# Kernel optimization log

Measured on AMD Instinct MI355X. Metric: run time of the kernel, lower is better.

The kernel has to match this reference:

```python
import jax, jax.numpy as jnp
import numpy as np

N = 50000
IN_C, HID, OUT_C = 128, 64, 40


def setup_inputs() -> dict:
    key = jax.random.key(0)
    ks = jax.random.split(key, 10)
    x = jax.random.normal(ks[0], (N, IN_C), dtype=jnp.float32)
    edge_index = jax.random.randint(ks[1], (2, 1600000), 0, N, dtype=jnp.int64)
    edge_attr = jax.random.uniform(ks[2], (1600000,), dtype=jnp.float32)
    def lin(k, fan_in, fan_out):
        bound = 1.0 / np.sqrt(fan_in)
        return jax.random.uniform(k, (fan_in, fan_out), jnp.float32, -bound, bound)
    W1 = lin(ks[3], IN_C, HID); b1 = jnp.zeros((HID,), jnp.float32)
    W2 = lin(ks[4], HID, HID); b2 = jnp.zeros((HID,), jnp.float32)
    W3 = lin(ks[5], HID, OUT_C); b3 = jnp.zeros((OUT_C,), jnp.float32)
    return {"x": x, "edge_index": edge_index, "edge_attr": edge_attr,
            "W1": W1, "b1": b1, "W2": W2, "b2": b2, "W3": W3, "b3": b3}


def _gcn_conv(x, src, dst, norm, W, b):
    # h = x W ; out[i] = sum_{(j->i)} norm_e * h[j] ; + bias
    h = x @ W
    msg = norm[:, None] * h[src]          # [E+N, F_out] gathered messages
    out = jax.ops.segment_sum(msg, dst, num_segments=N)
    return out + b


def reference(x, edge_index, edge_attr, W1, b1, W2, b2, W3, b3):
    # GCN normalization with self-loops (fill_value=1), cached across layers.
    loops = jnp.arange(N, dtype=edge_index.dtype)
    src = jnp.concatenate([edge_index[0], loops])
    dst = jnp.concatenate([edge_index[1], loops])
    w = jnp.concatenate([edge_attr, jnp.ones((N,), edge_attr.dtype)])
    deg = jnp.zeros((N,), x.dtype).at[dst].add(w)
    dinv = jnp.where(deg > 0, jax.lax.rsqrt(deg), 0.0)
    norm = dinv[src] * w * dinv[dst]

    h = jax.nn.relu(_gcn_conv(x, src, dst, norm, W1, b1))   # dropout: eval no-op
    h = jax.nn.relu(_gcn_conv(h, src, dst, norm, W2, b2))
    h = jax.nn.relu(_gcn_conv(h, src, dst, norm, W3, b3))
    return jax.nn.log_softmax(h, axis=-1)
```

## Files before the change

kernel.cpp:

```cpp
#include <hip/hip_runtime.h>
#include <math.h>

#define N_NODES 50000
#define E_EDGES 1600000
#define IN_C    128
#define HID     64
#define OUT_C   40

#define BSH     9
#define BNODES  512
#define NB      98
#define CAP     20480
#define TILE    4096
#define P1T     512
#define NPB     16

typedef unsigned int uint;
typedef unsigned short ushort;

__device__ inline float b2f(ushort h) { return __uint_as_float(((uint)h) << 16); }
__device__ inline ushort f2b(float f) {
    uint u = __float_as_uint(f);
    u += 0x7FFFu + ((u >> 16) & 1u);
    return (ushort)(u >> 16);
}

__global__ __launch_bounds__(P1T) void k_bin(const int* __restrict__ ei,
                                             const float* __restrict__ w,
                                             int* __restrict__ bcursor,
                                             uint2* __restrict__ tmp) {
    __shared__ uint2 stage[TILE];
    __shared__ unsigned char sbuck[TILE];
    __shared__ int hist[NB], startb[NB], cursor[NB], baseg[NB];
    __shared__ int sc[128];
    const int tid = threadIdx.x;
    const int e0  = blockIdx.x * TILE;
    const int n   = min(TILE, E_EDGES - e0);

    for (int i = tid; i < NB; i += P1T) hist[i] = 0;
    __syncthreads();

    for (int i = tid; i < n; i += P1T) {
        int d = ei[E_EDGES + e0 + i];
        atomicAdd(&hist[d >> BSH], 1);
    }
    __syncthreads();

    if (tid < 128) sc[tid] = (tid < NB) ? hist[tid] : 0;
    __syncthreads();
    for (int off = 1; off < 128; off <<= 1) {
        int x = 0;
        if (tid < 128 && tid >= off) x = sc[tid - off];
        __syncthreads();
        if (tid < 128) sc[tid] += x;
        __syncthreads();
    }
    if (tid < NB) {
        int st = sc[tid] - hist[tid];
        startb[tid] = st;
        cursor[tid] = st;
        baseg[tid]  = atomicAdd(&bcursor[tid], hist[tid]);
    }
    __syncthreads();

    for (int i = tid; i < n; i += P1T) {
        int   s  = ei[e0 + i];
        int   d  = ei[E_EDGES + e0 + i];
        float wv = w[e0 + i];
        int   b  = d >> BSH;
        int pos = atomicAdd(&cursor[b], 1);
        stage[pos] = make_uint2(((uint)(d & (BNODES - 1)) << 16) | (uint)s,
                                __float_as_uint(wv));
        sbuck[pos] = (unsigned char)b;
    }
    __syncthreads();

    for (int i = tid; i < n; i += P1T) {
        int b = sbuck[i];
        int gpos = baseg[b] + (i - startb[b]);
        tmp[(size_t)b * CAP + gpos] = stage[i];
    }
}

__global__ __launch_bounds__(BNODES) void k_build(const int* __restrict__ bcursor,
                                                  const uint2* __restrict__ tmp,
                                                  int* __restrict__ rowptr,
                                                  float* __restrict__ dinv,
                                                  uint* __restrict__ csr) {
    __shared__ int   hist[BNODES];
    __shared__ float wsum[BNODES];
    __shared__ int   sc[BNODES];
    __shared__ int   sb[128];
    __shared__ int   s_eb;
    const int tid = threadIdx.x;
    const int b   = blockIdx.x;

    if (tid < 128) sb[tid] = (tid < NB) ? bcursor[tid] : 0;
    hist[tid] = 0; wsum[tid] = 0.0f;
    __syncthreads();
    for (int off = 1; off < 128; off <<= 1) {
        int x = (tid < 128 && tid >= off) ? sb[tid - off] : 0;
        __syncthreads();
        if (tid < 128) sb[tid] += x;
        __syncthreads();
    }
    if (tid == 0) s_eb = sb[b] - bcursor[b];
    __syncthreads();
    const int cnt = bcursor[b];
    const int eb  = s_eb;
    const uint2* tb = tmp + (size_t)b * CAP;

    for (int i = tid; i < cnt; i += BNODES) {
        uint2 u = tb[i];
        int dl = u.x >> 16;
        atomicAdd(&hist[dl], 1);
        atomicAdd(&wsum[dl], __uint_as_float(u.y));
    }
    __syncthreads();

    int own = hist[tid];
    sc[tid] = own;
    __syncthreads();
    for (int off = 1; off < BNODES; off <<= 1) {
        int x = (tid >= off) ? sc[tid - off] : 0;
        __syncthreads();
        sc[tid] += x;
        __syncthreads();
    }
    int excl = sc[tid] - own;
    int node = (b << BSH) + tid;
    if (node < N_NODES) {
        rowptr[node] = eb + excl;
        dinv[node]   = rsqrtf(1.0f + wsum[tid]);
    }
    if (b == 0 && tid == 0) rowptr[N_NODES] = E_EDGES;
    hist[tid] = excl;
    __syncthreads();

    for (int i = tid; i < cnt; i += BNODES) {
        uint2 u = tb[i];
        int dl = u.x >> 16;
        int pos = atomicAdd(&hist[dl], 1);
        csr[eb + pos] = ((uint)f2b(__uint_as_float(u.y)) << 16) | (u.x & 0xFFFFu);
    }
}

__global__ __launch_bounds__(256) void k_gemm1(const float* __restrict__ x,
                                               const float* __restrict__ W,
                                               const float* __restrict__ dinv,
                                               ushort* __restrict__ g) {
    __shared__ float sW[IN_C * HID];
    __shared__ float sx[NPB * IN_C];
    const int tid = threadIdx.x;
    const size_t base = (size_t)blockIdx.x * NPB;

    for (int i = tid; i < (IN_C * HID) / 4; i += 256)
        ((float4*)sW)[i] = ((const float4*)W)[i];
    for (int i = tid; i < (NPB * IN_C) / 4; i += 256)
        ((float4*)sx)[i] = ((const float4*)(x + base * IN_C))[i];
    __syncthreads();

    const int wv = tid >> 6, f = tid & 63;
    for (int nn = 0; nn < 4; ++nn) {
        const int nl = wv * 4 + nn;
        const float* row = &sx[nl * IN_C];
        float acc = 0.0f;
#pragma unroll 8
        for (int k = 0; k < IN_C; k += 4) {
            float4 a = *(const float4*)&row[k];
            acc += a.x * sW[(k + 0) * HID + f] + a.y * sW[(k + 1) * HID + f]
                 + a.z * sW[(k + 2) * HID + f] + a.w * sW[(k + 3) * HID + f];
        }
        const size_t node = base + nl;
        g[node * HID + f] = f2b(dinv[node] * acc);
    }
}

template <int F_OUT>
__global__ __launch_bounds__(256) void k_agg_gemm(const int* __restrict__ rowptr,
                                                  const uint* __restrict__ csr,
                                                  const ushort* __restrict__ g,
                                                  const float* __restrict__ dinv,
                                                  const float* __restrict__ bias,
                                                  const float* __restrict__ W,
                                                  ushort* __restrict__ g_next) {
    __shared__ float sW[HID * F_OUT];
    __shared__ float s_act[4][HID];
    const int tid  = threadIdx.x;
    for (int i = tid; i < HID * F_OUT; i += 256) sW[i] = W[i];

    const int wv   = tid >> 6;
    const int lane = tid & 63;
    const int node = blockIdx.x * 4 + wv;
    const int grp  = lane >> 4;
    const int sub  = lane & 15;
    const int beg = rowptr[node], end = rowptr[node + 1];

    float4 acc0, acc1;
    acc0.x = acc0.y = acc0.z = acc0.w = 0.0f;
    acc1 = acc0;
    if (grp == 0) {
        ushort4 v = ((const ushort4*)(g + (size_t)node * HID))[sub];
        acc0.x = b2f(v.x); acc0.y = b2f(v.y); acc0.z = b2f(v.z); acc0.w = b2f(v.w);
    }

    uint curd = csr[min(beg + sub, E_EDGES - 1)];
    for (int e = beg; e < end; e += 16) {
        uint nextd = csr[min(e + 16 + sub, E_EDGES - 1)];
#pragma unroll
        for (int i = 0; i < 4; ++i) {
            uint d = __shfl(curd, (grp << 4) + 4 * i + grp);
            bool valid = (e + 4 * i + grp) < end;
            float wv2 = valid ? b2f((ushort)(d >> 16)) : 0.0f;
            int srcn = (int)(d & 0xFFFFu);
            ushort4 v = ((const ushort4*)(g + (size_t)srcn * HID))[sub];
            if (i & 1) {
                acc1.x += wv2 * b2f(v.x); acc1.y += wv2 * b2f(v.y);
                acc1.z += wv2 * b2f(v.z); acc1.w += wv2 * b2f(v.w);
            } else {
                acc0.x += wv2 * b2f(v.x); acc0.y += wv2 * b2f(v.y);
                acc0.z += wv2 * b2f(v.z); acc0.w += wv2 * b2f(v.w);
            }
        }
        curd = nextd;
    }
    acc0.x += acc1.x; acc0.y += acc1.y; acc0.z += acc1.z; acc0.w += acc1.w;
#pragma unroll
    for (int m = 16; m <= 32; m <<= 1) {
        acc0.x += __shfl_xor(acc0.x, m); acc0.y += __shfl_xor(acc0.y, m);
        acc0.z += __shfl_xor(acc0.z, m); acc0.w += __shfl_xor(acc0.w, m);
    }
    if (grp == 0) {
        float dv = dinv[node];
        float4 b4 = ((const float4*)bias)[sub];
        float4 v;
        v.x = fmaxf(dv * acc0.x + b4.x, 0.0f);
        v.y = fmaxf(dv * acc0.y + b4.y, 0.0f);
        v.z = fmaxf(dv * acc0.z + b4.z, 0.0f);
        v.w = fmaxf(dv * acc0.w + b4.w, 0.0f);
        ((float4*)&s_act[wv][0])[sub] = v;
    }
    __syncthreads();
    if (lane < F_OUT) {
        float dot = 0.0f;
#pragma unroll 4
        for (int k = 0; k < HID; k += 4) {
            float4 a = *(const float4*)&s_act[wv][k];
            dot += a.x * sW[(k + 0) * F_OUT + lane] + a.y * sW[(k + 1) * F_OUT + lane]
                 + a.z * sW[(k + 2) * F_OUT + lane] + a.w * sW[(k + 3) * F_OUT + lane];
        }
        g_next[(size_t)node * F_OUT + lane] = f2b(dinv[node] * dot);
    }
}

__global__ __launch_bounds__(256) void k_final_agg(const int* __restrict__ rowptr,
                                                   const uint* __restrict__ csr,
                                                   const ushort* __restrict__ g,
                                                   const float* __restrict__ dinv,
                                                   const float* __restrict__ bias,
                                                   float* __restrict__ out) {
    const int tid  = threadIdx.x;
    const int wv   = tid >> 6;
    const int lane = tid & 63;
    const int node = blockIdx.x * 4 + wv;
    const int grp  = lane >> 4;
    const int sub  = lane & 15;
    const bool live = sub < (OUT_C / 4);
    const int beg = rowptr[node], end = rowptr[node + 1];

    float4 acc0, acc1;
    acc0.x = acc0.y = acc0.z = acc0.w = 0.0f;
    acc1 = acc0;
    if (grp == 0 && live) {
        ushort4 v = ((const ushort4*)(g + (size_t)node * OUT_C))[sub];
        acc0.x = b2f(v.x); acc0.y = b2f(v.y); acc0.z = b2f(v.z); acc0.w = b2f(v.w);
    }

    uint curd = csr[min(beg + sub, E_EDGES - 1)];
    for (int e = beg; e < end; e += 16) {
        uint nextd = csr[min(e + 16 + sub, E_EDGES - 1)];
#pragma unroll
        for (int i = 0; i < 4; ++i) {
            uint d = __shfl(curd, (grp << 4) + 4 * i + grp);
            bool valid = (e + 4 * i + grp) < end;
            float wv2 = valid ? b2f((ushort)(d >> 16)) : 0.0f;
            int srcn = (int)(d & 0xFFFFu);
            if (live) {
                ushort4 v = ((const ushort4*)(g + (size_t)srcn * OUT_C))[sub];
                if (i & 1) {
                    acc1.x += wv2 * b2f(v.x); acc1.y += wv2 * b2f(v.y);
                    acc1.z += wv2 * b2f(v.z); acc1.w += wv2 * b2f(v.w);
                } else {
                    acc0.x += wv2 * b2f(v.x); acc0.y += wv2 * b2f(v.y);
                    acc0.z += wv2 * b2f(v.z); acc0.w += wv2 * b2f(v.w);
                }
            }
        }
        curd = nextd;
    }
    acc0.x += acc1.x; acc0.y += acc1.y; acc0.z += acc1.z; acc0.w += acc1.w;
#pragma unroll
    for (int m = 16; m <= 32; m <<= 1) {
        acc0.x += __shfl_xor(acc0.x, m); acc0.y += __shfl_xor(acc0.y, m);
        acc0.z += __shfl_xor(acc0.z, m); acc0.w += __shfl_xor(acc0.w, m);
    }

    float dv = dinv[node];
    float4 v; v.x = v.y = v.z = v.w = 0.0f;
    bool own = (grp == 0) && live;
    if (own) {
        float4 b4 = ((const float4*)bias)[sub];
        v.x = fmaxf(dv * acc0.x + b4.x, 0.0f);
        v.y = fmaxf(dv * acc0.y + b4.y, 0.0f);
        v.z = fmaxf(dv * acc0.z + b4.z, 0.0f);
        v.w = fmaxf(dv * acc0.w + b4.w, 0.0f);
    }
    float m = own ? fmaxf(fmaxf(v.x, v.y), fmaxf(v.z, v.w)) : -INFINITY;
#pragma unroll
    for (int off = 1; off < 16; off <<= 1) m = fmaxf(m, __shfl_xor(m, off));
    float s = own ? (expf(v.x - m) + expf(v.y - m) + expf(v.z - m) + expf(v.w - m)) : 0.0f;
#pragma unroll
    for (int off = 1; off < 16; off <<= 1) s += __shfl_xor(s, off);
    if (own) {
        float lg = m + logf(s);
        float4 o;
        o.x = v.x - lg; o.y = v.y - lg; o.z = v.z - lg; o.w = v.w - lg;
        ((float4*)&out[(size_t)node * OUT_C])[sub] = o;
    }
}

extern "C" void kernel_launch(void* const* d_in, const int* in_sizes, int n_in,
                              void* d_out, int out_size, void* d_ws, size_t ws_size,
                              hipStream_t stream) {
    const float* x  = (const float*)d_in[0];
    const int*   ei = (const int*)d_in[1];
    const float* w  = (const float*)d_in[2];
    const float* W1 = (const float*)d_in[3];
    const float* b1 = (const float*)d_in[4];
    const float* W2 = (const float*)d_in[5];
    const float* b2 = (const float*)d_in[6];
    const float* W3 = (const float*)d_in[7];
    const float* b3 = (const float*)d_in[8];
    float* out = (float*)d_out;

    char* ws = (char*)d_ws;
    size_t off = 0;
    auto carve = [&](size_t bytes) {
        char* p = ws + off;
        off += (bytes + 255) & ~(size_t)255;
        return p;
    };
    int*   bcursor = (int*)carve(NB * sizeof(int));
    int*   rowptr  = (int*)carve((N_NODES + 1) * sizeof(int));
    float* dinv    = (float*)carve(N_NODES * sizeof(float));
    uint*  csr     = (uint*)carve((size_t)E_EDGES * sizeof(uint));
    uint2* tmp     = (uint2*)carve((size_t)NB * CAP * sizeof(uint2));
    ushort* g1 = (ushort*)tmp;
    ushort* g2 = g1 + (size_t)N_NODES * HID;
    ushort* g3 = g1;
    (void)ws_size;

    const int nbBin = (E_EDGES + TILE - 1) / TILE;
    const int nbN4  = N_NODES / 4;
    const int nbG1  = N_NODES / NPB;

    hipMemsetAsync(bcursor, 0, NB * sizeof(int), stream);
    k_bin<<<nbBin, P1T, 0, stream>>>(ei, w, bcursor, tmp);
    k_build<<<NB, BNODES, 0, stream>>>(bcursor, tmp, rowptr, dinv, csr);

    k_gemm1<<<nbG1, 256, 0, stream>>>(x, W1, dinv, g1);
    k_agg_gemm<HID><<<nbN4, 256, 0, stream>>>(rowptr, csr, g1, dinv, b1, W2, g2);
    k_agg_gemm<OUT_C><<<nbN4, 256, 0, stream>>>(rowptr, csr, g2, dinv, b2, W3, g3);
    k_final_agg<<<nbN4, 256, 0, stream>>>(rowptr, csr, g3, dinv, b3, out);
}
```

Before: 253.6 us.

## Use 16-byte row gathers with two-deep prefetch in GCN aggregation kernels

Both aggregation kernels now assign 8 lanes per edge, and each lane loads a uint4 (8 bf16 values) instead of 16 lanes each loading a ushort4. Each wave therefore handles 8 edges per step. The edge loop is software-pipelined: the gathered neighbor rows for the next two 16-edge chunks are issued before the current chunk is accumulated, and the CSR entries are prefetched three chunks ahead. This aims to keep more outstanding memory requests in flight and hide gather latency, at the cost of more registers per thread. In the 40-wide final layer, non-live lanes also issue loads that read past the row end.

```diff
diff --git a/kernel.cpp b/kernel.cpp
--- a/kernel.cpp
+++ b/kernel.cpp
@@ -23,6 +23,27 @@
     uint u = __float_as_uint(f);
     u += 0x7FFFu + ((u >> 16) & 1u);
     return (ushort)(u >> 16);
+}
+#define BLO(u) __uint_as_float((u) << 16)
+#define BHI(u) __uint_as_float((u) & 0xFFFF0000u)
+#define FMA8(A, B, v, ww) do { \
+    (A).x += (ww) * BLO((v).x); (A).y += (ww) * BHI((v).x); \
+    (A).z += (ww) * BLO((v).y); (A).w += (ww) * BHI((v).y); \
+    (B).x += (ww) * BLO((v).z); (B).y += (ww) * BHI((v).z); \
+    (B).z += (ww) * BLO((v).w); (B).w += (ww) * BHI((v).w); } while (0)
+
+struct EV { uint4 a, b; float wa, wb; };
+
+template <int FW>
+__device__ __forceinline__ void issue_ev(uint dvec, int ebase, int end,
+                                         const ushort* __restrict__ g,
+                                         int grp, int sub, EV& E) {
+    uint d0 = __shfl(dvec, grp);
+    uint d1 = __shfl(dvec, 8 + grp);
+    E.wa = (ebase + grp     < end) ? b2f((ushort)(d0 >> 16)) : 0.0f;
+    E.wb = (ebase + 8 + grp < end) ? b2f((ushort)(d1 >> 16)) : 0.0f;
+    E.a = ((const uint4*)(g + (size_t)(d0 & 0xFFFFu) * FW))[sub];
+    E.b = ((const uint4*)(g + (size_t)(d1 & 0xFFFFu) * FW))[sub];
 }
 
 __global__ __launch_bounds__(P1T) void k_bin(const int* __restrict__ ei,
@@ -186,59 +207,56 @@
                                                   ushort* __restrict__ g_next) {
     __shared__ float sW[HID * F_OUT];
     __shared__ float s_act[4][HID];
-    const int tid  = threadIdx.x;
+    const int tid = threadIdx.x;
     for (int i = tid; i < HID * F_OUT; i += 256) sW[i] = W[i];
 
-    const int wv   = tid >> 6;
-    const int lane = tid & 63;
-    const int node = blockIdx.x * 4 + wv;
-    const int grp  = lane >> 4;
-    const int sub  = lane & 15;
+    const int wv = tid >> 6, lane = tid & 63;
+    const int node  = blockIdx.x * 4 + wv;
+    const int grp   = lane >> 3;
+    const int sub   = lane & 7;
+    const int dslot = lane & 15;
     const int beg = rowptr[node], end = rowptr[node + 1];
-
-    float4 acc0, acc1;
-    acc0.x = acc0.y = acc0.z = acc0.w = 0.0f;
-    acc1 = acc0;
+    const float dv = dinv[node];
+
+    float4 accA = {0.f, 0.f, 0.f, 0.f}, accB = accA;
     if (grp == 0) {
-        ushort4 v = ((const ushort4*)(g + (size_t)node * HID))[sub];
-        acc0.x = b2f(v.x); acc0.y = b2f(v.y); acc0.z = b2f(v.z); acc0.w = b2f(v.w);
-    }
-
-    uint curd = csr[min(beg + sub, E_EDGES - 1)];
-    for (int e = beg; e < end; e += 16) {
-        uint nextd = csr[min(e + 16 + sub, E_EDGES - 1)];
+        uint4 v = ((const uint4*)(g + (size_t)node * HID))[sub];
+        accA.x = BLO(v.x); accA.y = BHI(v.x); accA.z = BLO(v.y); accA.w = BHI(v.y);
+        accB.x = BLO(v.z); accB.y = BHI(v.z); accB.z = BLO(v.w); accB.w = BHI(v.w);
+    }
+
+    if (beg < end) {
+        uint dv0 = csr[min(beg      + dslot, E_EDGES - 1)];
+        uint dv1 = csr[min(beg + 16 + dslot, E_EDGES - 1)];
+        uint dv2 = csr[min(beg + 32 + dslot, E_EDGES - 1)];
+        EV E0, E1, En;
+        issue_ev<HID>(dv0, beg,      end, g, grp, sub, E0);
+        issue_ev<HID>(dv1, beg + 16, end, g, grp, sub, E1);
+        for (int e = beg; e < end; e += 16) {
+            issue_ev<HID>(dv2, e + 32, end, g, grp, sub, En);
+            dv2 = csr[min(e + 48 + dslot, E_EDGES - 1)];
+            FMA8(accA, accB, E0.a, E0.wa);
+            FMA8(accA, accB, E0.b, E0.wb);
+            E0 = E1; E1 = En;
+        }
+    }
 #pragma unroll
-        for (int i = 0; i < 4; ++i) {
-            uint d = __shfl(curd, (grp << 4) + 4 * i + grp);
-            bool valid = (e + 4 * i + grp) < end;
-            float wv2 = valid ? b2f((ushort)(d >> 16)) : 0.0f;
-            int srcn = (int)(d & 0xFFFFu);
-            ushort4 v = ((const ushort4*)(g + (size_t)srcn * HID))[sub];
-            if (i & 1) {
-                acc1.x += wv2 * b2f(v.x); acc1.y += wv2 * b2f(v.y);
-                acc1.z += wv2 * b2f(v.z); acc1.w += wv2 * b2f(v.w);
-            } else {
-                acc0.x += wv2 * b2f(v.x); acc0.y += wv2 * b2f(v.y);
-                acc0.z += wv2 * b2f(v.z); acc0.w += wv2 * b2f(v.w);
-            }
-        }
-        curd = nextd;
-    }
-    acc0.x += acc1.x; acc0.y += acc1.y; acc0.z += acc1.z; acc0.w += acc1.w;
-#pragma unroll
-    for (int m = 16; m <= 32; m <<= 1) {
-        acc0.x += __shfl_xor(acc0.x, m); acc0.y += __shfl_xor(acc0.y, m);
-        acc0.z += __shfl_xor(acc0.z, m); acc0.w += __shfl_xor(acc0.w, m);
+    for (int m = 8; m <= 32; m <<= 1) {
+        accA.x += __shfl_xor(accA.x, m); accA.y += __shfl_xor(accA.y, m);
+        accA.z += __shfl_xor(accA.z, m); accA.w += __shfl_xor(accA.w, m);
+        accB.x += __shfl_xor(accB.x, m); accB.y += __shfl_xor(accB.y, m);
+        accB.z += __shfl_xor(accB.z, m); accB.w += __shfl_xor(accB.w, m);
     }
     if (grp == 0) {
-        float dv = dinv[node];
-        float4 b4 = ((const float4*)bias)[sub];
-        float4 v;
-        v.x = fmaxf(dv * acc0.x + b4.x, 0.0f);
-        v.y = fmaxf(dv * acc0.y + b4.y, 0.0f);
-        v.z = fmaxf(dv * acc0.z + b4.z, 0.0f);
-        v.w = fmaxf(dv * acc0.w + b4.w, 0.0f);
-        ((float4*)&s_act[wv][0])[sub] = v;
+        float4 bA = ((const float4*)bias)[2 * sub];
+        float4 bB = ((const float4*)bias)[2 * sub + 1];
+        float4 rA, rB;
+        rA.x = fmaxf(dv * accA.x + bA.x, 0.f); rA.y = fmaxf(dv * accA.y + bA.y, 0.f);
+        rA.z = fmaxf(dv * accA.z + bA.z, 0.f); rA.w = fmaxf(dv * accA.w + bA.w, 0.f);
+        rB.x = fmaxf(dv * accB.x + bB.x, 0.f); rB.y = fmaxf(dv * accB.y + bB.y, 0.f);
+        rB.z = fmaxf(dv * accB.z + bB.z, 0.f); rB.w = fmaxf(dv * accB.w + bB.w, 0.f);
+        ((float4*)&s_act[wv][0])[2 * sub]     = rA;
+        ((float4*)&s_act[wv][0])[2 * sub + 1] = rB;
     }
     __syncthreads();
     if (lane < F_OUT) {
@@ -259,73 +277,71 @@
                                                    const float* __restrict__ dinv,
                                                    const float* __restrict__ bias,
                                                    float* __restrict__ out) {
-    const int tid  = threadIdx.x;
-    const int wv   = tid >> 6;
-    const int lane = tid & 63;
-    const int node = blockIdx.x * 4 + wv;
-    const int grp  = lane >> 4;
-    const int sub  = lane & 15;
-    const bool live = sub < (OUT_C / 4);
+    const int tid = threadIdx.x;
+    const int wv = tid >> 6, lane = tid & 63;
+    const int node  = blockIdx.x * 4 + wv;
+    const int grp   = lane >> 3;
+    const int sub   = lane & 7;
+    const int dslot = lane & 15;
+    const bool live = sub < (OUT_C / 8);
     const int beg = rowptr[node], end = rowptr[node + 1];
-
-    float4 acc0, acc1;
-    acc0.x = acc0.y = acc0.z = acc0.w = 0.0f;
-    acc1 = acc0;
+    const float dv = dinv[node];
+
+    float4 accA = {0.f, 0.f, 0.f, 0.f}, accB = accA;
     if (grp == 0 && live) {
-        ushort4 v = ((const ushort4*)(g + (size_t)node * OUT_C))[sub];
-        acc0.x = b2f(v.x); acc0.y = b2f(v.y); acc0.z = b2f(v.z); acc0.w = b2f(v.w);
-    }
-
-    uint curd = csr[min(beg + sub, E_EDGES - 1)];
-    for (int e = beg; e < end; e += 16) {
-        uint nextd = csr[min(e + 16 + sub, E_EDGES - 1)];
+        uint4 v = ((const uint4*)(g + (size_t)node * OUT_C))[sub];
+        accA.x = BLO(v.x); accA.y = BHI(v.x); accA.z = BLO(v.y); accA.w = BHI(v.y);
+        accB.x = BLO(v.z); accB.y = BHI(v.z); accB.z = BLO(v.w); accB.w = BHI(v.w);
+    }
+
+    if (beg < end) {
+        uint dv0 = csr[min(beg      + dslot, E_EDGES - 1)];
+        uint dv1 = csr[min(beg + 16 + dslot, E_EDGES - 1)];
+        uint dv2 = csr[min(beg + 32 + dslot, E_EDGES - 1)];
+        EV E0, E1, En;
+        issue_ev<OUT_C>(dv0, beg,      end, g, grp, sub, E0);
+        issue_ev<OUT_C>(dv1, beg + 16, end, g, grp, sub, E1);
+        for (int e = beg; e < end; e += 16) {
+            issue_ev<OUT_C>(dv2, e + 32, end, g, grp, sub, En);
+            dv2 = csr[min(e + 48 + dslot, E_EDGES - 1)];
+            FMA8(accA, accB, E0.a, E0.wa);
+            FMA8(accA, accB, E0.b, E0.wb);
+            E0 = E1; E1 = En;
+        }
+    }
 #pragma unroll
-        for (int i = 0; i < 4; ++i) {
-            uint d = __shfl(curd, (grp << 4) + 4 * i + grp);
-            bool valid = (e + 4 * i + grp) < end;
-            float wv2 = valid ? b2f((ushort)(d >> 16)) : 0.0f;
-            int srcn = (int)(d & 0xFFFFu);
-            if (live) {
-                ushort4 v = ((const ushort4*)(g + (size_t)srcn * OUT_C))[sub];
-                if (i & 1) {
-                    acc1.x += wv2 * b2f(v.x); acc1.y += wv2 * b2f(v.y);
-                    acc1.z += wv2 * b2f(v.z); acc1.w += wv2 * b2f(v.w);
-                } else {
-                    acc0.x += wv2 * b2f(v.x); acc0.y += wv2 * b2f(v.y);
-                    acc0.z += wv2 * b2f(v.z); acc0.w += wv2 * b2f(v.w);
-                }
-            }
-        }
-        curd = nextd;
-    }
-    acc0.x += acc1.x; acc0.y += acc1.y; acc0.z += acc1.z; acc0.w += acc1.w;
+    for (int m = 8; m <= 32; m <<= 1) {
+        accA.x += __shfl_xor(accA.x, m); accA.y += __shfl_xor(accA.y, m);
+        accA.z += __shfl_xor(accA.z, m); accA.w += __shfl_xor(accA.w, m);
+        accB.x += __shfl_xor(accB.x, m); accB.y += __shfl_xor(accB.y, m);
+        accB.z += __shfl_xor(accB.z, m); accB.w += __shfl_xor(accB.w, m);
+    }
+
+    const bool own = (grp == 0) && live;
+    float4 vA = {0.f, 0.f, 0.f, 0.f}, vB = vA;
+    if (own) {
+        float4 bA = ((const float4*)bias)[2 * sub];
+        float4 bB = ((const float4*)bias)[2 * sub + 1];
+        vA.x = fmaxf(dv * accA.x + bA.x, 0.f); vA.y = fmaxf(dv * accA.y + bA.y, 0.f);
+        vA.z = fmaxf(dv * accA.z + bA.z, 0.f); vA.w = fmaxf(dv * accA.w + bA.w, 0.f);
+        vB.x = fmaxf(dv * accB.x + bB.x, 0.f); vB.y = fmaxf(dv * accB.y + bB.y, 0.f);
+        vB.z = fmaxf(dv * accB.z + bB.z, 0.f); vB.w = fmaxf(dv * accB.w + bB.w, 0.f);
+    }
+    float mx = own ? fmaxf(fmaxf(fmaxf(vA.x, vA.y), fmaxf(vA.z, vA.w)),
+                           fmaxf(fmaxf(vB.x, vB.y), fmaxf(vB.z, vB.w))) : -INFINITY;
 #pragma unroll
-    for (int m = 16; m <= 32; m <<= 1) {
-        acc0.x += __shfl_xor(acc0.x, m); acc0.y += __shfl_xor(acc0.y, m);
-        acc0.z += __shfl_xor(acc0.z, m); acc0.w += __shfl_xor(acc0.w, m);
-    }
-
-    float dv = dinv[node];
-    float4 v; v.x = v.y = v.z = v.w = 0.0f;
-    bool own = (grp == 0) && live;
+    for (int off = 1; off < 8; off <<= 1) mx = fmaxf(mx, __shfl_xor(mx, off));
+    float se = own ? (expf(vA.x - mx) + expf(vA.y - mx) + expf(vA.z - mx) + expf(vA.w - mx)
+                    + expf(vB.x - mx) + expf(vB.y - mx) + expf(vB.z - mx) + expf(vB.w - mx)) : 0.f;
+#pragma unroll
+    for (int off = 1; off < 8; off <<= 1) se += __shfl_xor(se, off);
     if (own) {
-        float4 b4 = ((const float4*)bias)[sub];
-        v.x = fmaxf(dv * acc0.x + b4.x, 0.0f);
-        v.y = fmaxf(dv * acc0.y + b4.y, 0.0f);
-        v.z = fmaxf(dv * acc0.z + b4.z, 0.0f);
-        v.w = fmaxf(dv * acc0.w + b4.w, 0.0f);
-    }
-    float m = own ? fmaxf(fmaxf(v.x, v.y), fmaxf(v.z, v.w)) : -INFINITY;
-#pragma unroll
-    for (int off = 1; off < 16; off <<= 1) m = fmaxf(m, __shfl_xor(m, off));
-    float s = own ? (expf(v.x - m) + expf(v.y - m) + expf(v.z - m) + expf(v.w - m)) : 0.0f;
-#pragma unroll
-    for (int off = 1; off < 16; off <<= 1) s += __shfl_xor(s, off);
-    if (own) {
-        float lg = m + logf(s);
-        float4 o;
-        o.x = v.x - lg; o.y = v.y - lg; o.z = v.z - lg; o.w = v.w - lg;
-        ((float4*)&out[(size_t)node * OUT_C])[sub] = o;
+        float lg = mx + logf(se);
+        float4 oA, oB;
+        oA.x = vA.x - lg; oA.y = vA.y - lg; oA.z = vA.z - lg; oA.w = vA.w - lg;
+        oB.x = vB.x - lg; oB.y = vB.y - lg; oB.z = vB.z - lg; oB.w = vB.w - lg;
+        ((float4*)(out + (size_t)node * OUT_C))[2 * sub]     = oA;
+        ((float4*)(out + (size_t)node * OUT_C))[2 * sub + 1] = oB;
     }
 }
 
```

Measured after the change: 247.1 us. -2.6%, faster.
